# Performance work log

Measured on AMD Instinct MI355X. Metric: run time of the kernel, lower is better.

The kernel has to match this reference:

```python
import jax, jax.numpy as jnp
import numpy as np

B = 65536
H = 256
STEPS = 128


def setup_inputs() -> dict:
    key = jax.random.key(0)
    ks = jax.random.split(key, 6)
    scale = 0.1
    return {
        "x": jax.random.normal(ks[0], (B, H), dtype=jnp.float32),
        "W_hh": jax.random.normal(ks[1], (H, H), dtype=jnp.float32) * scale,
        "fc1_w": jax.random.normal(ks[2], (H, H), dtype=jnp.float32) * (1.0 / np.sqrt(H)),
        "fc1_b": jax.random.normal(ks[3], (H,), dtype=jnp.float32) * 0.01,
        "fc2_w": jax.random.normal(ks[4], (H, H), dtype=jnp.float32) * (1.0 / np.sqrt(H)),
        "fc2_b": jax.random.normal(ks[5], (H,), dtype=jnp.float32) * 0.01,
        "steps": STEPS,
    }


def reference(x, W_hh, fc1_w, fc1_b, fc2_w, fc2_b, steps):
    # h = fc1(x)  (torch Linear: x @ W.T + b)
    h0 = x @ fc1_w.T + fc1_b

    def step(h, _):
        return jnp.tanh(h @ W_hh), None

    h, _ = jax.lax.scan(step, h0, None, length=steps)
    out = h @ fc2_w.T + fc2_b
    return (out, h)
```

## Files before the change

### kernel.cpp

```cpp
#include <hip/hip_runtime.h>
#include <math.h>

#define Hd 256
#define BM 64
#define KP 16
#define NP 16
#define THREADS 512
#define HLD 68
#define WLD 260

__device__ __forceinline__ float tanh_xla(float x) {
    const float plus_clamp = 7.90531110763549805f;
    float xc = fminf(fmaxf(x, -plus_clamp), plus_clamp);
    float x2 = xc * xc;
    float p = fmaf(x2, -2.76076847742355e-16f, 2.00018790482477e-13f);
    p = fmaf(x2, p, -8.60467152213735e-11f);
    p = fmaf(x2, p,  5.12229709037114e-08f);
    p = fmaf(x2, p,  1.48572235717979e-05f);
    p = fmaf(x2, p,  6.37261928875436e-04f);
    p = fmaf(x2, p,  4.89352455891786e-03f);
    p = xc * p;
    float q = fmaf(x2, 1.19825839466702e-06f, 1.18534705686654e-04f);
    q = fmaf(x2, q, 2.26843463243900e-03f);
    q = fmaf(x2, q, 4.89352518554385e-03f);
    float r = p / q;
    return (fabsf(x) < 0.0004f) ? x : r;
}

__global__ __launch_bounds__(THREADS, 1)
void rnn_fused(const float* __restrict__ x, const float* __restrict__ Whh,
               const float* __restrict__ fc1w, const float* __restrict__ fc1b,
               const float* __restrict__ fc2w, const float* __restrict__ fc2b,
               float* __restrict__ outF, float* __restrict__ hF) {
    __shared__ __align__(16) float Hs[Hd][HLD];
    __shared__ __align__(16) float Wp[2][KP][WLD];

    const int  t    = threadIdx.x;
    const long row0 = (long)blockIdx.x * BM;
    const int  tm   = t & 15;
    const int  tn   = t >> 4;

    {
        const int ar = t >> 3;
        const int aq = t & 7;
        const float* xb = x + (row0 + ar) * Hd + aq * 4;
#pragma unroll
        for (int q = 0; q < 8; ++q) {
            float4 v = *reinterpret_cast<const float4*>(xb + q * 32);
            const int k = q * 32 + aq * 4;
            Hs[k + 0][ar] = v.x;
            Hs[k + 1][ar] = v.y;
            Hs[k + 2][ar] = v.z;
            Hs[k + 3][ar] = v.w;
        }
    }
    __syncthreads();

    float acc[4][8];

    const int wk = t >> 5;
    const int wn = (t & 31) * 8;
    const int vn = t >> 1;
    const int vk = (t & 1) * 8;

    float4 r0, r1;

    auto wload_nt = [&](int p) {
        const float* b = Whh + (long)(p * KP + wk) * Hd + wn;
        r0 = *reinterpret_cast<const float4*>(b);
        r1 = *reinterpret_cast<const float4*>(b + 4);
    };
    auto wstore_nt = [&](int buf) {
        *reinterpret_cast<float4*>(&Wp[buf][wk][wn])     = r0;
        *reinterpret_cast<float4*>(&Wp[buf][wk][wn + 4]) = r1;
    };
    auto wload_t = [&](const float* W, int p) {
        const float* b = W + (long)vn * Hd + p * KP + vk;
        r0 = *reinterpret_cast<const float4*>(b);
        r1 = *reinterpret_cast<const float4*>(b + 4);
    };
    auto wstore_t = [&](int buf) {
        const float* f0 = reinterpret_cast<const float*>(&r0);
        const float* f1 = reinterpret_cast<const float*>(&r1);
#pragma unroll
        for (int i = 0; i < 4; ++i) Wp[buf][vk + i][vn]     = f0[i];
#pragma unroll
        for (int i = 0; i < 4; ++i) Wp[buf][vk + 4 + i][vn] = f1[i];
    };

    auto zero_acc = [&]() {
#pragma unroll
        for (int i = 0; i < 4; ++i)
#pragma unroll
            for (int j = 0; j < 8; ++j) acc[i][j] = 0.f;
    };

    auto compute_panel = [&](int buf, int kbase) {
#pragma unroll 2
        for (int kk = 0; kk < KP; ++kk) {
            float4 av = *reinterpret_cast<const float4*>(&Hs[kbase + kk][tm * 4]);
            float4 wa = *reinterpret_cast<const float4*>(&Wp[buf][kk][tn * 8]);
            float4 wb = *reinterpret_cast<const float4*>(&Wp[buf][kk][tn * 8 + 4]);
            const float aa[4] = {av.x, av.y, av.z, av.w};
            const float ww[8] = {wa.x, wa.y, wa.z, wa.w, wb.x, wb.y, wb.z, wb.w};
#pragma unroll
            for (int i = 0; i < 4; ++i)
#pragma unroll
                for (int j = 0; j < 8; ++j)
                    acc[i][j] = fmaf(aa[i], ww[j], acc[i][j]);
        }
    };

    auto run_nt = [&]() {
        zero_acc();
        wload_nt(0); wstore_nt(0);
        __syncthreads();
#pragma unroll 1
        for (int p = 0; p < NP; ++p) {
            if (p + 1 < NP) wload_nt(p + 1);
            compute_panel(p & 1, p * KP);
            if (p + 1 < NP) wstore_nt((p + 1) & 1);
            __syncthreads();
        }
    };
    auto run_t = [&](const float* W) {
        zero_acc();
        wload_t(W, 0); wstore_t(0);
        __syncthreads();
#pragma unroll 1
        for (int p = 0; p < NP; ++p) {
            if (p + 1 < NP) wload_t(W, p + 1);
            compute_panel(p & 1, p * KP);
            if (p + 1 < NP) wstore_t((p + 1) & 1);
            __syncthreads();
        }
    };

    auto writeback_h = [&]() {
#pragma unroll
        for (int j = 0; j < 8; ++j)
            *reinterpret_cast<float4*>(&Hs[tn * 8 + j][tm * 4]) =
                make_float4(acc[0][j], acc[1][j], acc[2][j], acc[3][j]);
    };

    run_t(fc1w);
#pragma unroll
    for (int j = 0; j < 8; ++j) {
        float bj = fc1b[tn * 8 + j];
#pragma unroll
        for (int i = 0; i < 4; ++i) acc[i][j] += bj;
    }
    writeback_h();
    __syncthreads();

#pragma unroll 1
    for (int s = 0; s < 128; ++s) {
        run_nt();
#pragma unroll
        for (int i = 0; i < 4; ++i)
#pragma unroll
            for (int j = 0; j < 8; ++j)
                acc[i][j] = tanh_xla(acc[i][j]);
        writeback_h();
        __syncthreads();
    }

#pragma unroll
    for (int i = 0; i < 4; ++i) {
        const long r = row0 + tm * 4 + i;
        *reinterpret_cast<float4*>(&hF[r * Hd + tn * 8]) =
            make_float4(acc[i][0], acc[i][1], acc[i][2], acc[i][3]);
        *reinterpret_cast<float4*>(&hF[r * Hd + tn * 8 + 4]) =
            make_float4(acc[i][4], acc[i][5], acc[i][6], acc[i][7]);
    }

    run_t(fc2w);
#pragma unroll
    for (int j = 0; j < 8; ++j) {
        float bj = fc2b[tn * 8 + j];
#pragma unroll
        for (int i = 0; i < 4; ++i) acc[i][j] += bj;
    }
#pragma unroll
    for (int i = 0; i < 4; ++i) {
        const long r = row0 + tm * 4 + i;
        *reinterpret_cast<float4*>(&outF[r * Hd + tn * 8]) =
            make_float4(acc[i][0], acc[i][1], acc[i][2], acc[i][3]);
        *reinterpret_cast<float4*>(&outF[r * Hd + tn * 8 + 4]) =
            make_float4(acc[i][4], acc[i][5], acc[i][6], acc[i][7]);
    }
}

extern "C" void kernel_launch(void* const* d_in, const int* in_sizes, int n_in,
                              void* d_out, int out_size, void* d_ws, size_t ws_size,
                              hipStream_t stream) {
    const float* x     = (const float*)d_in[0];
    const float* W_hh  = (const float*)d_in[1];
    const float* fc1_w = (const float*)d_in[2];
    const float* fc1_b = (const float*)d_in[3];
    const float* fc2_w = (const float*)d_in[4];
    const float* fc2_b = (const float*)d_in[5];

    const int B = in_sizes[0] / Hd;
    float* out = (float*)d_out;
    float* h   = out + (long)B * Hd;

    rnn_fused<<<dim3(B / BM), dim3(THREADS), 0, stream>>>(
        x, W_hh, fc1_w, fc1_b, fc2_w, fc2_b, out, h);
}
```

Before: 15.19 ms.

## Double rows per block to reuse each weight panel across two hidden tiles

Each block now handles 128 batch rows split into two 64-row shared-memory tiles. Every W_hh panel loaded from global memory feeds twice as many FMAs, and each thread holds 64 accumulators instead of 32. To fit the second hidden tile in LDS, the weight panel drops from double to single buffering, which adds an extra barrier per panel. The grid is halved to 512 blocks, and higher register pressure could cause spills or reduce overlap.

```diff
diff --git a/kernel.cpp b/kernel.cpp
--- a/kernel.cpp
+++ b/kernel.cpp
@@ -2,7 +2,7 @@
 #include <math.h>
 
 #define Hd 256
-#define BM 64
+#define BM 128
 #define KP 16
 #define NP 16
 #define THREADS 512
@@ -32,8 +32,9 @@
                const float* __restrict__ fc1w, const float* __restrict__ fc1b,
                const float* __restrict__ fc2w, const float* __restrict__ fc2b,
                float* __restrict__ outF, float* __restrict__ hF) {
-    __shared__ __align__(16) float Hs[Hd][HLD];
-    __shared__ __align__(16) float Wp[2][KP][WLD];
+    __shared__ __align__(16) float Hs0[Hd][HLD];
+    __shared__ __align__(16) float Hs1[Hd][HLD];
+    __shared__ __align__(16) float Wp[KP][WLD];
 
     const int  t    = threadIdx.x;
     const long row0 = (long)blockIdx.x * BM;
@@ -41,153 +42,184 @@
     const int  tn   = t >> 4;
 
     {
-        const int ar = t >> 3;
-        const int aq = t & 7;
-        const float* xb = x + (row0 + ar) * Hd + aq * 4;
-#pragma unroll
-        for (int q = 0; q < 8; ++q) {
-            float4 v = *reinterpret_cast<const float4*>(xb + q * 32);
-            const int k = q * 32 + aq * 4;
-            Hs[k + 0][ar] = v.x;
-            Hs[k + 1][ar] = v.y;
-            Hs[k + 2][ar] = v.z;
-            Hs[k + 3][ar] = v.w;
+        const int r  = t >> 2;
+        const int kq = (t & 3) * 4;
+        float (*H)[HLD] = (r < 64) ? Hs0 : Hs1;
+        const int m = r & 63;
+        const float* src = x + (row0 + r) * Hd + kq;
+#pragma unroll
+        for (int q = 0; q < 16; ++q) {
+            float4 v = *reinterpret_cast<const float4*>(src + q * 16);
+            const int k = q * 16 + kq;
+            H[k + 0][m] = v.x;
+            H[k + 1][m] = v.y;
+            H[k + 2][m] = v.z;
+            H[k + 3][m] = v.w;
         }
     }
     __syncthreads();
 
-    float acc[4][8];
-
-    const int wk = t >> 5;
-    const int wn = (t & 31) * 8;
-    const int vn = t >> 1;
-    const int vk = (t & 1) * 8;
-
-    float4 r0, r1;
-
-    auto wload_nt = [&](int p) {
-        const float* b = Whh + (long)(p * KP + wk) * Hd + wn;
-        r0 = *reinterpret_cast<const float4*>(b);
-        r1 = *reinterpret_cast<const float4*>(b + 4);
-    };
-    auto wstore_nt = [&](int buf) {
-        *reinterpret_cast<float4*>(&Wp[buf][wk][wn])     = r0;
-        *reinterpret_cast<float4*>(&Wp[buf][wk][wn + 4]) = r1;
-    };
-    auto wload_t = [&](const float* W, int p) {
-        const float* b = W + (long)vn * Hd + p * KP + vk;
-        r0 = *reinterpret_cast<const float4*>(b);
-        r1 = *reinterpret_cast<const float4*>(b + 4);
-    };
-    auto wstore_t = [&](int buf) {
-        const float* f0 = reinterpret_cast<const float*>(&r0);
-        const float* f1 = reinterpret_cast<const float*>(&r1);
-#pragma unroll
-        for (int i = 0; i < 4; ++i) Wp[buf][vk + i][vn]     = f0[i];
-#pragma unroll
-        for (int i = 0; i < 4; ++i) Wp[buf][vk + 4 + i][vn] = f1[i];
+    float accL[4][8], accH[4][8];
+    float4 pf0, pf1;
+
+    auto ld_nt = [&](const float* W, int p) {
+        const int k0 = p * KP;
+        int c0 = t;           int wk0 = c0 >> 6, wn0 = c0 & 63;
+        int c1 = 512 + t;     int wk1 = c1 >> 6, wn1 = c1 & 63;
+        pf0 = *reinterpret_cast<const float4*>(W + (long)(k0 + wk0) * Hd + wn0 * 4);
+        pf1 = *reinterpret_cast<const float4*>(W + (long)(k0 + wk1) * Hd + wn1 * 4);
+    };
+    auto st_nt = [&]() {
+        int c0 = t;           int wk0 = c0 >> 6, wn0 = c0 & 63;
+        int c1 = 512 + t;     int wk1 = c1 >> 6, wn1 = c1 & 63;
+        *reinterpret_cast<float4*>(&Wp[wk0][wn0 * 4]) = pf0;
+        *reinterpret_cast<float4*>(&Wp[wk1][wn1 * 4]) = pf1;
+    };
+    auto ld_t = [&](const float* W, int p) {
+        const int k0 = p * KP;
+        int c0 = t;           int n0 = c0 >> 2, kq0 = (c0 & 3) * 4;
+        int c1 = 512 + t;     int n1 = c1 >> 2, kq1 = (c1 & 3) * 4;
+        pf0 = *reinterpret_cast<const float4*>(W + (long)n0 * Hd + k0 + kq0);
+        pf1 = *reinterpret_cast<const float4*>(W + (long)n1 * Hd + k0 + kq1);
+    };
+    auto st_t = [&]() {
+        int c0 = t;           int n0 = c0 >> 2, kq0 = (c0 & 3) * 4;
+        int c1 = 512 + t;     int n1 = c1 >> 2, kq1 = (c1 & 3) * 4;
+        const float* f0 = reinterpret_cast<const float*>(&pf0);
+        const float* f1 = reinterpret_cast<const float*>(&pf1);
+#pragma unroll
+        for (int i = 0; i < 4; ++i) Wp[kq0 + i][n0] = f0[i];
+#pragma unroll
+        for (int i = 0; i < 4; ++i) Wp[kq1 + i][n1] = f1[i];
     };
 
     auto zero_acc = [&]() {
 #pragma unroll
         for (int i = 0; i < 4; ++i)
 #pragma unroll
-            for (int j = 0; j < 8; ++j) acc[i][j] = 0.f;
-    };
-
-    auto compute_panel = [&](int buf, int kbase) {
+            for (int j = 0; j < 8; ++j) { accL[i][j] = 0.f; accH[i][j] = 0.f; }
+    };
+
+    auto compute_panel = [&](int kbase) {
 #pragma unroll 2
         for (int kk = 0; kk < KP; ++kk) {
-            float4 av = *reinterpret_cast<const float4*>(&Hs[kbase + kk][tm * 4]);
-            float4 wa = *reinterpret_cast<const float4*>(&Wp[buf][kk][tn * 8]);
-            float4 wb = *reinterpret_cast<const float4*>(&Wp[buf][kk][tn * 8 + 4]);
-            const float aa[4] = {av.x, av.y, av.z, av.w};
-            const float ww[8] = {wa.x, wa.y, wa.z, wa.w, wb.x, wb.y, wb.z, wb.w};
+            float4 aL = *reinterpret_cast<const float4*>(&Hs0[kbase + kk][tm * 4]);
+            float4 aH = *reinterpret_cast<const float4*>(&Hs1[kbase + kk][tm * 4]);
+            float4 w0 = *reinterpret_cast<const float4*>(&Wp[kk][tn * 8]);
+            float4 w1 = *reinterpret_cast<const float4*>(&Wp[kk][tn * 8 + 4]);
+            const float al[4] = {aL.x, aL.y, aL.z, aL.w};
+            const float ah[4] = {aH.x, aH.y, aH.z, aH.w};
+            const float ww[8] = {w0.x, w0.y, w0.z, w0.w, w1.x, w1.y, w1.z, w1.w};
 #pragma unroll
             for (int i = 0; i < 4; ++i)
 #pragma unroll
-                for (int j = 0; j < 8; ++j)
-                    acc[i][j] = fmaf(aa[i], ww[j], acc[i][j]);
-        }
-    };
-
-    auto run_nt = [&]() {
+                for (int j = 0; j < 8; ++j) {
+                    accL[i][j] = fmaf(al[i], ww[j], accL[i][j]);
+                    accH[i][j] = fmaf(ah[i], ww[j], accH[i][j]);
+                }
+        }
+    };
+
+    auto run_nt = [&](const float* W) {
         zero_acc();
-        wload_nt(0); wstore_nt(0);
+        ld_nt(W, 0); st_nt();
         __syncthreads();
 #pragma unroll 1
         for (int p = 0; p < NP; ++p) {
-            if (p + 1 < NP) wload_nt(p + 1);
-            compute_panel(p & 1, p * KP);
-            if (p + 1 < NP) wstore_nt((p + 1) & 1);
+            const bool more = (p + 1 < NP);
+            if (more) ld_nt(W, p + 1);
+            compute_panel(p * KP);
             __syncthreads();
+            if (more) { st_nt(); __syncthreads(); }
         }
     };
     auto run_t = [&](const float* W) {
         zero_acc();
-        wload_t(W, 0); wstore_t(0);
+        ld_t(W, 0); st_t();
         __syncthreads();
 #pragma unroll 1
         for (int p = 0; p < NP; ++p) {
-            if (p + 1 < NP) wload_t(W, p + 1);
-            compute_panel(p & 1, p * KP);
-            if (p + 1 < NP) wstore_t((p + 1) & 1);
+            const bool more = (p + 1 < NP);
+            if (more) ld_t(W, p + 1);
+            compute_panel(p * KP);
             __syncthreads();
+            if (more) { st_t(); __syncthreads(); }
         }
     };
 
     auto writeback_h = [&]() {
 #pragma unroll
-        for (int j = 0; j < 8; ++j)
-            *reinterpret_cast<float4*>(&Hs[tn * 8 + j][tm * 4]) =
-                make_float4(acc[0][j], acc[1][j], acc[2][j], acc[3][j]);
+        for (int j = 0; j < 8; ++j) {
+            *reinterpret_cast<float4*>(&Hs0[tn * 8 + j][tm * 4]) =
+                make_float4(accL[0][j], accL[1][j], accL[2][j], accL[3][j]);
+            *reinterpret_cast<float4*>(&Hs1[tn * 8 + j][tm * 4]) =
+                make_float4(accH[0][j], accH[1][j], accH[2][j], accH[3][j]);
+        }
     };
 
     run_t(fc1w);
-#pragma unroll
-    for (int j = 0; j < 8; ++j) {
-        float bj = fc1b[tn * 8 + j];
-#pragma unroll
-        for (int i = 0; i < 4; ++i) acc[i][j] += bj;
+    {
+        float4 b0 = *reinterpret_cast<const float4*>(fc1b + tn * 8);
+        float4 b1 = *reinterpret_cast<const float4*>(fc1b + tn * 8 + 4);
+        const float bj[8] = {b0.x, b0.y, b0.z, b0.w, b1.x, b1.y, b1.z, b1.w};
+#pragma unroll
+        for (int i = 0; i < 4; ++i)
+#pragma unroll
+            for (int j = 0; j < 8; ++j) { accL[i][j] += bj[j]; accH[i][j] += bj[j]; }
     }
     writeback_h();
     __syncthreads();
 
 #pragma unroll 1
     for (int s = 0; s < 128; ++s) {
-        run_nt();
-#pragma unroll
-        for (int i = 0; i < 4; ++i)
-#pragma unroll
-            for (int j = 0; j < 8; ++j)
-                acc[i][j] = tanh_xla(acc[i][j]);
+        run_nt(Whh);
+#pragma unroll
+        for (int i = 0; i < 4; ++i)
+#pragma unroll
+            for (int j = 0; j < 8; ++j) {
+                accL[i][j] = tanh_xla(accL[i][j]);
+                accH[i][j] = tanh_xla(accH[i][j]);
+            }
         writeback_h();
         __syncthreads();
     }
 
 #pragma unroll
     for (int i = 0; i < 4; ++i) {
-        const long r = row0 + tm * 4 + i;
-        *reinterpret_cast<float4*>(&hF[r * Hd + tn * 8]) =
-            make_float4(acc[i][0], acc[i][1], acc[i][2], acc[i][3]);
-        *reinterpret_cast<float4*>(&hF[r * Hd + tn * 8 + 4]) =
-            make_float4(acc[i][4], acc[i][5], acc[i][6], acc[i][7]);
+        const long rL = row0 + tm * 4 + i;
+        const long rH = rL + 64;
+        *reinterpret_cast<float4*>(&hF[rL * Hd + tn * 8]) =
+            make_float4(accL[i][0], accL[i][1], accL[i][2], accL[i][3]);
+        *reinterpret_cast<float4*>(&hF[rL * Hd + tn * 8 + 4]) =
+            make_float4(accL[i][4], accL[i][5], accL[i][6], accL[i][7]);
+        *reinterpret_cast<float4*>(&hF[rH * Hd + tn * 8]) =
+            make_float4(accH[i][0], accH[i][1], accH[i][2], accH[i][3]);
+        *reinterpret_cast<float4*>(&hF[rH * Hd + tn * 8 + 4]) =
+            make_float4(accH[i][4], accH[i][5], accH[i][6], accH[i][7]);
     }
 
     run_t(fc2w);
-#pragma unroll
-    for (int j = 0; j < 8; ++j) {
-        float bj = fc2b[tn * 8 + j];
-#pragma unroll
-        for (int i = 0; i < 4; ++i) acc[i][j] += bj;
+    {
+        float4 b0 = *reinterpret_cast<const float4*>(fc2b + tn * 8);
+        float4 b1 = *reinterpret_cast<const float4*>(fc2b + tn * 8 + 4);
+        const float bj[8] = {b0.x, b0.y, b0.z, b0.w, b1.x, b1.y, b1.z, b1.w};
+#pragma unroll
+        for (int i = 0; i < 4; ++i)
+#pragma unroll
+            for (int j = 0; j < 8; ++j) { accL[i][j] += bj[j]; accH[i][j] += bj[j]; }
     }
 #pragma unroll
     for (int i = 0; i < 4; ++i) {
-        const long r = row0 + tm * 4 + i;
-        *reinterpret_cast<float4*>(&outF[r * Hd + tn * 8]) =
-            make_float4(acc[i][0], acc[i][1], acc[i][2], acc[i][3]);
-        *reinterpret_cast<float4*>(&outF[r * Hd + tn * 8 + 4]) =
-            make_float4(acc[i][4], acc[i][5], acc[i][6], acc[i][7]);
+        const long rL = row0 + tm * 4 + i;
+        const long rH = rL + 64;
+        *reinterpret_cast<float4*>(&outF[rL * Hd + tn * 8]) =
+            make_float4(accL[i][0], accL[i][1], accL[i][2], accL[i][3]);
+        *reinterpret_cast<float4*>(&outF[rL * Hd + tn * 8 + 4]) =
+            make_float4(accL[i][4], accL[i][5], accL[i][6], accL[i][7]);
+        *reinterpret_cast<float4*>(&outF[rH * Hd + tn * 8]) =
+            make_float4(accH[i][0], accH[i][1], accH[i][2], accH[i][3]);
+        *reinterpret_cast<float4*>(&outF[rH * Hd + tn * 8 + 4]) =
+            make_float4(accH[i][4], accH[i][5], accH[i][6], accH[i][7]);
     }
 }
 
```

New measurement: 13.31 ms. -12.3%, faster.
